# Kernel optimization log

Hardware: AMD Instinct MI355X
Metric: run time of the kernel (lower is better)

Reference implementation:

```python
import jax, jax.numpy as jnp
import numpy as np

N_S, N_T = 64, 32
N_EFF = N_S * N_T          # 2048
K_T1, K_T2 = 8, 8
BATCH = 16


def _orthonormal(key, n):
    q, _ = jnp.linalg.qr(jax.random.normal(key, (n, n), dtype=jnp.float32))
    return q.astype(jnp.float32)


def setup_inputs() -> dict:
    key = jax.random.key(0)
    ks = jax.random.split(key, 6)
    return {
        "s_effective_batch": jax.random.normal(ks[0], (BATCH, N_EFF), dtype=jnp.float32),
        "U_G": _orthonormal(ks[1], N_S),
        "U_P_T": _orthonormal(ks[2], N_T),
        "h0": jax.random.normal(ks[3], (N_EFF,), dtype=jnp.float32) * 0.01,
        "h_hat_1_coeffs": jax.random.normal(ks[4], (N_S, K_T1), dtype=jnp.float32) * 0.01,
        "H_hat_2_S": jax.random.normal(ks[5], (N_S, N_S), dtype=jnp.float32) * 0.01,
        "H_hat_2_T_coeffs": jax.random.normal(jax.random.fold_in(key, 7), (K_T2, K_T2), dtype=jnp.float32) * 0.01,
    }


def reference(s_effective_batch, U_G, U_P_T, h0, h_hat_1_coeffs, H_hat_2_S, H_hat_2_T_coeffs):
    # spatio-temporal basis via Kronecker product: [N_eff, N_eff]
    U_ST = jnp.kron(U_G, U_P_T)

    # GFT as in the module: s_hat = s @ U_ST
    s_hat = s_effective_batch @ U_ST                       # [B, N_eff]

    # linear (first-order Volterra) term
    Ub1 = U_P_T[:, :K_T1]                                  # [N_T, K1]
    full_h_hat_1 = (h_hat_1_coeffs @ Ub1.T).reshape(-1)    # [N_eff]
    z1 = (full_h_hat_1[None, :] * s_hat) @ U_ST            # iGFT as in module: @ U_ST

    # quadratic kernel H2 = kron(H2_S, Ub2 @ C @ Ub2^T)
    Ub2 = U_P_T[:, :K_T2]
    full_H2_T = Ub2 @ (H_hat_2_T_coeffs @ Ub2.T)           # [N_T, N_T]
    H2 = jnp.kron(H_hat_2_S, full_H2_T)                    # [N_eff, N_eff]

    # z2[b,i] = diag( U_ST (H2 * s_hat_b s_hat_b^T) U_ST^T )_i
    #         = sum_{k,l} B[b,i,k] H2[k,l] B[b,i,l], with B[b,i,k] = U_ST[i,k]*s_hat[b,k]
    B = U_ST[None, :, :] * s_hat[:, None, :]               # [B, N_eff, N_eff]
    z2 = jnp.einsum('bik,kl,bil->bi', B, H2, B)            # batched GEMM + row-reduce

    return h0[None, :] + z1 + z2
```

## Files before the change

### kernel.cpp

```cpp
#include <hip/hip_runtime.h>


typedef short  bf16x8 __attribute__((ext_vector_type(8)));
typedef float  f32x4  __attribute__((ext_vector_type(4)));

static __device__ __forceinline__ unsigned short f2bf(float f) {
  unsigned u = __float_as_uint(f);
  u = (u + 0x7fff + ((u >> 16) & 1)) >> 16;
  return (unsigned short)u;
}
static __device__ __forceinline__ float bf2f(unsigned short h) {
  return __uint_as_float(((unsigned)h) << 16);
}
static __device__ __forceinline__ float dot4(f32x4 a, f32x4 b) {
  return a.x * b.x + a.y * b.y + a.z * b.z + a.w * b.w;
}

__global__ __launch_bounds__(256) void volterra_one(
    const float* __restrict__ s, const float* __restrict__ UG,
    const float* __restrict__ UPT, const float* __restrict__ h0,
    const float* __restrict__ h1c, const float* __restrict__ HS,
    const float* __restrict__ Hc, float* __restrict__ out)
{
  const int b  = blockIdx.x >> 5;
  const int iT = blockIdx.x & 31;
  const int t  = threadIdx.x;
  const int w  = t >> 6;
  const int l  = t & 63;
  const int r  = l & 15;
  const int g  = l >> 4;

  __shared__ __align__(16) float sS[64][36];
  __shared__ __align__(16) float sT1E[2304];
  __shared__ __align__(16) unsigned short sUGh[4096];
  __shared__ __align__(16) unsigned short sUPTTh[32 * 40];
  __shared__ __align__(16) unsigned short sUPTTl[32 * 40];
  __shared__ float sUPT[32][33];
  __shared__ float sUhc[32 * 9];
  __shared__ float sh1c[512];
  __shared__ __align__(16) float wGm[8 * 36];
  __shared__ __align__(16) float wA[8 * 36];
  __shared__ __align__(16) float wQ[8 * 36];
  __shared__ __align__(16) float sGm[64][12];
  __shared__ __align__(16) float sA[64][12];
  __shared__ float wv[64];
  __shared__ float zp1[4][64];
  __shared__ float zpart[4][64];

  for (int o = t; o < 2048; o += 256) sS[o >> 5][o & 31] = s[b * 2048 + o];
  for (int o = t; o < 1024; o += 256) {
    const int k = o >> 5, c = o & 31;
    const float f = UPT[o];
    sUPT[k][c] = f;
    const unsigned short hi = f2bf(f);
    sUPTTh[c * 40 + k] = hi;
    sUPTTl[c * 40 + k] = f2bf(f - bf2f(hi));
  }
  for (int o = t; o < 4096; o += 256) {
    const int rr = o >> 6, c = o & 63;
    sUGh[rr * 64 + (c ^ ((rr & 7) << 3))] = f2bf(UG[o]);
  }
  for (int o = t; o < 512; o += 256) sh1c[o] = h1c[o];
  {
    const int k = t >> 3, p = t & 7;
    float a = 0.f;
    #pragma unroll
    for (int q = 0; q < 8; ++q) a += UPT[k * 32 + q] * Hc[q * 8 + p];
    sUhc[k * 9 + p] = a;
  }
  __syncthreads();

  {
    const int p = t >> 5, k = t & 31;
    const float uiT_row = sUPT[iT][k];
    const float uiT_col = sUPT[k][iT];
    wGm[p * 36 + k] = uiT_row * sUPT[k][p];
    wA [p * 36 + k] = uiT_row * sUhc[k * 9 + p];
    wQ [p * 36 + k] = uiT_col * sUPT[k][p];
  }
  {
    f32x4 acc0 = {0.f, 0.f, 0.f, 0.f}, acc1 = {0.f, 0.f, 0.f, 0.f};
    #pragma unroll
    for (int kc = 0; kc < 2; ++kc) {
      float av[8];
      #pragma unroll
      for (int j = 0; j < 8; ++j)
        av[j] = UG[(kc * 32 + g * 8 + j) * 64 + 16 * w + r];
      bf16x8 Ah, Al;
      #pragma unroll
      for (int j = 0; j < 8; ++j) {
        const unsigned short hi = f2bf(av[j]);
        Ah[j] = (short)hi;
        Al[j] = (short)f2bf(av[j] - bf2f(hi));
      }
      #pragma unroll
      for (int ct = 0; ct < 2; ++ct) {
        float bv[8];
        #pragma unroll
        for (int j = 0; j < 8; ++j)
          bv[j] = sS[kc * 32 + g * 8 + j][ct * 16 + r];
        bf16x8 Bh, Bl;
        #pragma unroll
        for (int j = 0; j < 8; ++j) {
          const unsigned short hi = f2bf(bv[j]);
          Bh[j] = (short)hi;
          Bl[j] = (short)f2bf(bv[j] - bf2f(hi));
        }
        f32x4& acc = ct ? acc1 : acc0;
        acc = __builtin_amdgcn_mfma_f32_16x16x32_bf16(Ah, Bh, acc, 0, 0, 0);
        acc = __builtin_amdgcn_mfma_f32_16x16x32_bf16(Ah, Bl, acc, 0, 0, 0);
        acc = __builtin_amdgcn_mfma_f32_16x16x32_bf16(Al, Bh, acc, 0, 0, 0);
      }
    }
    #pragma unroll
    for (int reg = 0; reg < 4; ++reg) {
      sT1E[(16 * w + 4 * g + reg) * 36 + r]      = acc0[reg];
      sT1E[(16 * w + 4 * g + reg) * 36 + 16 + r] = acc1[reg];
    }
  }
  __syncthreads();

  {
    f32x4 av0 = *(const f32x4*)&sT1E[(16 * w + r) * 36 + g * 8];
    f32x4 av1 = *(const f32x4*)&sT1E[(16 * w + r) * 36 + g * 8 + 4];
    float av[8] = {av0.x, av0.y, av0.z, av0.w, av1.x, av1.y, av1.z, av1.w};
    bf16x8 Ah, Al;
    #pragma unroll
    for (int j = 0; j < 8; ++j) {
      const unsigned short hi = f2bf(av[j]);
      Ah[j] = (short)hi;
      Al[j] = (short)f2bf(av[j] - bf2f(hi));
    }
    f32x4 acc0 = {0.f, 0.f, 0.f, 0.f}, acc1 = {0.f, 0.f, 0.f, 0.f};
    #pragma unroll
    for (int ct = 0; ct < 2; ++ct) {
      const bf16x8 Bh = *(const bf16x8*)&sUPTTh[(ct * 16 + r) * 40 + g * 8];
      const bf16x8 Bl = *(const bf16x8*)&sUPTTl[(ct * 16 + r) * 40 + g * 8];
      f32x4& acc = ct ? acc1 : acc0;
      acc = __builtin_amdgcn_mfma_f32_16x16x32_bf16(Ah, Bh, acc, 0, 0, 0);
      acc = __builtin_amdgcn_mfma_f32_16x16x32_bf16(Ah, Bl, acc, 0, 0, 0);
      acc = __builtin_amdgcn_mfma_f32_16x16x32_bf16(Al, Bh, acc, 0, 0, 0);
    }
    __syncthreads();
    #pragma unroll
    for (int reg = 0; reg < 4; ++reg) {
      sS[16 * w + 4 * g + reg][r]      = acc0[reg];
      sS[16 * w + 4 * g + reg][16 + r] = acc1[reg];
    }
  }
  __syncthreads();

  {
    const int kSa = t >> 3, p = t & 7;
    float g0 = 0.f, g1v = 0.f, a0 = 0.f, a1v = 0.f, q0 = 0.f, q1v = 0.f;
    #pragma unroll
    for (int c4 = 0; c4 < 8; ++c4) {
      const f32x4 w1 = *(const f32x4*)&wGm[p * 36 + c4 * 4];
      const f32x4 w2 = *(const f32x4*)&wA [p * 36 + c4 * 4];
      const f32x4 w3 = *(const f32x4*)&wQ [p * 36 + c4 * 4];
      const f32x4 x0 = *(const f32x4*)&sS[kSa][c4 * 4];
      const f32x4 x1 = *(const f32x4*)&sS[kSa + 32][c4 * 4];
      g0  += dot4(x0, w1); a0  += dot4(x0, w2); q0  += dot4(x0, w3);
      g1v += dot4(x1, w1); a1v += dot4(x1, w2); q1v += dot4(x1, w3);
    }
    sGm[kSa][p] = g0; sGm[kSa + 32][p] = g1v;
    sA [kSa][p] = a0; sA [kSa + 32][p] = a1v;
    float wv0 = sh1c[kSa * 8 + p] * q0;
    float wv1 = sh1c[(kSa + 32) * 8 + p] * q1v;
    wv0 += __shfl_xor(wv0, 1); wv0 += __shfl_xor(wv0, 2); wv0 += __shfl_xor(wv0, 4);
    wv1 += __shfl_xor(wv1, 1); wv1 += __shfl_xor(wv1, 2); wv1 += __shfl_xor(wv1, 4);
    if (p == 0) { wv[kSa] = wv0; wv[kSa + 32] = wv1; }
  }
  __syncthreads();

  {
    unsigned short* sEbf = (unsigned short*)sT1E;
    const f32x4 gr0 = *(const f32x4*)&sGm[l][0];
    const f32x4 gr1 = *(const f32x4*)&sGm[l][4];
    #pragma unroll 4
    for (int j = 0; j < 16; ++j) {
      const int kS = 4 * j + w;
      const f32x4 a0v = *(const f32x4*)&sA[kS][0];
      const f32x4 a1v = *(const f32x4*)&sA[kS][4];
      const float e = (dot4(a0v, gr0) + dot4(a1v, gr1)) * HS[kS * 64 + l];
      sEbf[kS * 64 + (l ^ ((kS & 7) << 3))] = f2bf(e);
    }
    const float wvl = wv[l];
    float part = 0.f;
    #pragma unroll
    for (int j = 0; j < 16; ++j) {
      const int kk = 16 * w + j;
      part += __shfl(wvl, kk) * UG[kk * 64 + l];
    }
    zp1[w][l] = part;
  }
  __syncthreads();

  {
    const unsigned short* sEbf = (const unsigned short*)sT1E;
    f32x4 acc[4];
    #pragma unroll
    for (int nt = 0; nt < 4; ++nt) acc[nt] = (f32x4){0.f, 0.f, 0.f, 0.f};
    #pragma unroll
    for (int ks = 0; ks < 2; ++ks) {
      const int kcol = g * 8 + ks * 32;
      const int rowA = 16 * w + r;
      const bf16x8 ah = *(const bf16x8*)&sEbf[rowA * 64 + (kcol ^ ((rowA & 7) << 3))];
      #pragma unroll
      for (int nt = 0; nt < 4; ++nt) {
        const int rowB = 16 * nt + r;
        const bf16x8 bh = *(const bf16x8*)&sUGh[rowB * 64 + (kcol ^ ((rowB & 7) << 3))];
        acc[nt] = __builtin_amdgcn_mfma_f32_16x16x32_bf16(ah, bh, acc[nt], 0, 0, 0);
      }
    }
    #pragma unroll
    for (int nt = 0; nt < 4; ++nt) {
      float zp = 0.f;
      #pragma unroll
      for (int reg = 0; reg < 4; ++reg) {
        const int kS = 16 * w + 4 * g + reg;
        const int iS = 16 * nt + r;
        zp += bf2f(sUGh[iS * 64 + (kS ^ ((iS & 7) << 3))]) * acc[nt][reg];
      }
      zp += __shfl_xor(zp, 16);
      zp += __shfl_xor(zp, 32);
      if (g == 0) zpart[w][16 * nt + r] = zp;
    }
  }
  __syncthreads();

  if (t < 64) {
    const float z2 = zpart[0][t] + zpart[1][t] + zpart[2][t] + zpart[3][t];
    const float z1 = zp1[0][t] + zp1[1][t] + zp1[2][t] + zp1[3][t];
    const int col = t * 32 + iT;
    out[b * 2048 + col] = h0[col] + z1 + z2;
  }
}

extern "C" void kernel_launch(void* const* d_in, const int* in_sizes, int n_in,
                              void* d_out, int out_size, void* d_ws, size_t ws_size,
                              hipStream_t stream) {
  const float* s   = (const float*)d_in[0];
  const float* UG  = (const float*)d_in[1];
  const float* UPT = (const float*)d_in[2];
  const float* h0  = (const float*)d_in[3];
  const float* h1c = (const float*)d_in[4];
  const float* HS  = (const float*)d_in[5];
  const float* Hc  = (const float*)d_in[6];
  float* out = (float*)d_out;

  volterra_one<<<512, 256, 0, stream>>>(s, UG, UPT, h0, h1c, HS, Hc, out);
}
```

Baseline: 14.78 us.

## Process two temporal indices per block to share GFT work across halves

Each block now handles two iT columns with 512 threads, halving the grid to 256 blocks. The shared s_hat computation (two MFMA GEMM stages) is split across 8 waves instead of recomputed per iT. Later stages run per side in parallel. Global loads are vectorized, and HS is staged in shared memory. This reduces redundant per-block prologue and GEMM work, at the cost of more LDS per block and fewer blocks (256 on a ~256-CU part, so about one block per CU).

```diff
diff --git a/kernel.cpp b/kernel.cpp
--- a/kernel.cpp
+++ b/kernel.cpp
@@ -3,66 +3,80 @@
 
 typedef short  bf16x8 __attribute__((ext_vector_type(8)));
 typedef float  f32x4  __attribute__((ext_vector_type(4)));
-
-static __device__ __forceinline__ unsigned short f2bf(float f) {
+typedef unsigned short u16;
+
+static __device__ __forceinline__ u16 f2bf(float f) {
   unsigned u = __float_as_uint(f);
   u = (u + 0x7fff + ((u >> 16) & 1)) >> 16;
-  return (unsigned short)u;
-}
-static __device__ __forceinline__ float bf2f(unsigned short h) {
+  return (u16)u;
+}
+static __device__ __forceinline__ float bf2f(u16 h) {
   return __uint_as_float(((unsigned)h) << 16);
 }
 static __device__ __forceinline__ float dot4(f32x4 a, f32x4 b) {
   return a.x * b.x + a.y * b.y + a.z * b.z + a.w * b.w;
 }
 
-__global__ __launch_bounds__(256) void volterra_one(
+__global__ __launch_bounds__(512) void volterra_one(
     const float* __restrict__ s, const float* __restrict__ UG,
     const float* __restrict__ UPT, const float* __restrict__ h0,
     const float* __restrict__ h1c, const float* __restrict__ HS,
     const float* __restrict__ Hc, float* __restrict__ out)
 {
-  const int b  = blockIdx.x >> 5;
-  const int iT = blockIdx.x & 31;
-  const int t  = threadIdx.x;
-  const int w  = t >> 6;
-  const int l  = t & 63;
-  const int r  = l & 15;
-  const int g  = l >> 4;
+  const int b   = blockIdx.x >> 4;
+  const int iT0 = (blockIdx.x & 15) << 1;
+  const int t   = threadIdx.x;
+  const int w   = t >> 6;
+  const int l   = t & 63;
+  const int r   = l & 15;
+  const int g   = l >> 4;
 
   __shared__ __align__(16) float sS[64][36];
-  __shared__ __align__(16) float sT1E[2304];
-  __shared__ __align__(16) unsigned short sUGh[4096];
-  __shared__ __align__(16) unsigned short sUPTTh[32 * 40];
-  __shared__ __align__(16) unsigned short sUPTTl[32 * 40];
-  __shared__ float sUPT[32][33];
+  __shared__ __align__(16) float sT1[64][36];
+  __shared__ __align__(16) u16   sUGh[4096];
+  __shared__ __align__(16) u16   sUPTTh[32 * 40];
+  __shared__ __align__(16) u16   sUPTTl[32 * 40];
+  __shared__ __align__(16) float sUPT[32][36];
+  __shared__ __align__(16) float sHS[64][68];
   __shared__ float sUhc[32 * 9];
-  __shared__ float sh1c[512];
-  __shared__ __align__(16) float wGm[8 * 36];
-  __shared__ __align__(16) float wA[8 * 36];
-  __shared__ __align__(16) float wQ[8 * 36];
-  __shared__ __align__(16) float sGm[64][12];
-  __shared__ __align__(16) float sA[64][12];
-  __shared__ float wv[64];
-  __shared__ float zp1[4][64];
-  __shared__ float zpart[4][64];
-
-  for (int o = t; o < 2048; o += 256) sS[o >> 5][o & 31] = s[b * 2048 + o];
-  for (int o = t; o < 1024; o += 256) {
-    const int k = o >> 5, c = o & 31;
-    const float f = UPT[o];
-    sUPT[k][c] = f;
-    const unsigned short hi = f2bf(f);
-    sUPTTh[c * 40 + k] = hi;
-    sUPTTl[c * 40 + k] = f2bf(f - bf2f(hi));
-  }
-  for (int o = t; o < 4096; o += 256) {
-    const int rr = o >> 6, c = o & 63;
-    sUGh[rr * 64 + (c ^ ((rr & 7) << 3))] = f2bf(UG[o]);
-  }
-  for (int o = t; o < 512; o += 256) sh1c[o] = h1c[o];
-  {
-    const int k = t >> 3, p = t & 7;
+  __shared__ __align__(16) float wGm[2][8 * 36], wA[2][8 * 36], wQ[2][8 * 36];
+  __shared__ __align__(16) float sGm[2][64][12], sA[2][64][12];
+  __shared__ __align__(16) u16   sE[2][4096];
+  __shared__ float wv[2][64];
+  __shared__ float zp1[2][4][64];
+  __shared__ float zpart[2][4][64];
+
+  {
+    const f32x4 v = ((const f32x4*)(s + b * 2048))[t];
+    *(f32x4*)&sS[t >> 3][(t & 7) * 4] = v;
+  }
+  #pragma unroll
+  for (int o4 = t, it = 0; it < 2; ++it, o4 += 512) {
+    const int rr = o4 >> 4, c0 = (o4 & 15) * 4;
+    const f32x4 v = ((const f32x4*)UG)[o4];
+    short4 h;
+    h.x = (short)f2bf(v.x); h.y = (short)f2bf(v.y);
+    h.z = (short)f2bf(v.z); h.w = (short)f2bf(v.w);
+    *(short4*)&sUGh[rr * 64 + (c0 ^ ((rr & 7) << 3))] = h;
+  }
+  #pragma unroll
+  for (int o4 = t, it = 0; it < 2; ++it, o4 += 512) {
+    const int rr = o4 >> 4, c0 = (o4 & 15) * 4;
+    *(f32x4*)&sHS[rr][c0] = ((const f32x4*)HS)[o4];
+  }
+  if (t < 256) {
+    const int k = t >> 3, c4 = t & 7;
+    const f32x4 v = ((const f32x4*)UPT)[t];
+    *(f32x4*)&sUPT[k][c4 * 4] = v;
+    float arr[4] = {v.x, v.y, v.z, v.w};
+    #pragma unroll
+    for (int i = 0; i < 4; ++i) {
+      const int c = 4 * c4 + i;
+      const u16 hi = f2bf(arr[i]);
+      sUPTTh[c * 40 + k] = hi;
+      sUPTTl[c * 40 + k] = f2bf(arr[i] - bf2f(hi));
+    }
+    const int p = t & 7;
     float a = 0.f;
     #pragma unroll
     for (int q = 0; q < 8; ++q) a += UPT[k * 32 + q] * Hc[q * 8 + p];
@@ -71,141 +85,125 @@
   __syncthreads();
 
   {
-    const int p = t >> 5, k = t & 31;
-    const float uiT_row = sUPT[iT][k];
-    const float uiT_col = sUPT[k][iT];
-    wGm[p * 36 + k] = uiT_row * sUPT[k][p];
-    wA [p * 36 + k] = uiT_row * sUhc[k * 9 + p];
-    wQ [p * 36 + k] = uiT_col * sUPT[k][p];
-  }
-  {
-    f32x4 acc0 = {0.f, 0.f, 0.f, 0.f}, acc1 = {0.f, 0.f, 0.f, 0.f};
+    const int side = t >> 8, p = (t >> 5) & 7, k = t & 31;
+    const int iTs = iT0 + side;
+    const float m1 = sUPT[iTs][k];
+    const float m3 = sUPT[k][iTs];
+    const float m2 = sUPT[k][p];
+    wGm[side][p * 36 + k] = m1 * m2;
+    wA [side][p * 36 + k] = m1 * sUhc[k * 9 + p];
+    wQ [side][p * 36 + k] = m3 * m2;
+  }
+  {
+    const int band = w >> 1, ct = w & 1;
+    f32x4 acc = {0.f, 0.f, 0.f, 0.f};
     #pragma unroll
     for (int kc = 0; kc < 2; ++kc) {
-      float av[8];
+      float av[8], bv[8];
       #pragma unroll
       for (int j = 0; j < 8; ++j)
-        av[j] = UG[(kc * 32 + g * 8 + j) * 64 + 16 * w + r];
-      bf16x8 Ah, Al;
+        av[j] = UG[(kc * 32 + g * 8 + j) * 64 + 16 * band + r];
+      #pragma unroll
+      for (int j = 0; j < 8; ++j)
+        bv[j] = sS[kc * 32 + g * 8 + j][ct * 16 + r];
+      bf16x8 Ah, Al, Bh, Bl;
       #pragma unroll
       for (int j = 0; j < 8; ++j) {
-        const unsigned short hi = f2bf(av[j]);
-        Ah[j] = (short)hi;
-        Al[j] = (short)f2bf(av[j] - bf2f(hi));
+        u16 h = f2bf(av[j]);
+        Ah[j] = (short)h; Al[j] = (short)f2bf(av[j] - bf2f(h));
+        h = f2bf(bv[j]);
+        Bh[j] = (short)h; Bl[j] = (short)f2bf(bv[j] - bf2f(h));
       }
-      #pragma unroll
-      for (int ct = 0; ct < 2; ++ct) {
-        float bv[8];
-        #pragma unroll
-        for (int j = 0; j < 8; ++j)
-          bv[j] = sS[kc * 32 + g * 8 + j][ct * 16 + r];
-        bf16x8 Bh, Bl;
-        #pragma unroll
-        for (int j = 0; j < 8; ++j) {
-          const unsigned short hi = f2bf(bv[j]);
-          Bh[j] = (short)hi;
-          Bl[j] = (short)f2bf(bv[j] - bf2f(hi));
-        }
-        f32x4& acc = ct ? acc1 : acc0;
-        acc = __builtin_amdgcn_mfma_f32_16x16x32_bf16(Ah, Bh, acc, 0, 0, 0);
-        acc = __builtin_amdgcn_mfma_f32_16x16x32_bf16(Ah, Bl, acc, 0, 0, 0);
-        acc = __builtin_amdgcn_mfma_f32_16x16x32_bf16(Al, Bh, acc, 0, 0, 0);
-      }
-    }
-    #pragma unroll
-    for (int reg = 0; reg < 4; ++reg) {
-      sT1E[(16 * w + 4 * g + reg) * 36 + r]      = acc0[reg];
-      sT1E[(16 * w + 4 * g + reg) * 36 + 16 + r] = acc1[reg];
-    }
-  }
-  __syncthreads();
-
-  {
-    f32x4 av0 = *(const f32x4*)&sT1E[(16 * w + r) * 36 + g * 8];
-    f32x4 av1 = *(const f32x4*)&sT1E[(16 * w + r) * 36 + g * 8 + 4];
-    float av[8] = {av0.x, av0.y, av0.z, av0.w, av1.x, av1.y, av1.z, av1.w};
-    bf16x8 Ah, Al;
-    #pragma unroll
-    for (int j = 0; j < 8; ++j) {
-      const unsigned short hi = f2bf(av[j]);
-      Ah[j] = (short)hi;
-      Al[j] = (short)f2bf(av[j] - bf2f(hi));
-    }
-    f32x4 acc0 = {0.f, 0.f, 0.f, 0.f}, acc1 = {0.f, 0.f, 0.f, 0.f};
-    #pragma unroll
-    for (int ct = 0; ct < 2; ++ct) {
-      const bf16x8 Bh = *(const bf16x8*)&sUPTTh[(ct * 16 + r) * 40 + g * 8];
-      const bf16x8 Bl = *(const bf16x8*)&sUPTTl[(ct * 16 + r) * 40 + g * 8];
-      f32x4& acc = ct ? acc1 : acc0;
       acc = __builtin_amdgcn_mfma_f32_16x16x32_bf16(Ah, Bh, acc, 0, 0, 0);
       acc = __builtin_amdgcn_mfma_f32_16x16x32_bf16(Ah, Bl, acc, 0, 0, 0);
       acc = __builtin_amdgcn_mfma_f32_16x16x32_bf16(Al, Bh, acc, 0, 0, 0);
     }
-    __syncthreads();
-    #pragma unroll
-    for (int reg = 0; reg < 4; ++reg) {
-      sS[16 * w + 4 * g + reg][r]      = acc0[reg];
-      sS[16 * w + 4 * g + reg][16 + r] = acc1[reg];
-    }
-  }
-  __syncthreads();
-
-  {
-    const int kSa = t >> 3, p = t & 7;
+    #pragma unroll
+    for (int reg = 0; reg < 4; ++reg)
+      sT1[16 * band + 4 * g + reg][ct * 16 + r] = acc[reg];
+  }
+  __syncthreads();
+
+  {
+    const int band = w >> 1, ct = w & 1;
+    const f32x4 a0 = *(const f32x4*)&sT1[16 * band + r][g * 8];
+    const f32x4 a1 = *(const f32x4*)&sT1[16 * band + r][g * 8 + 4];
+    float av[8] = {a0.x, a0.y, a0.z, a0.w, a1.x, a1.y, a1.z, a1.w};
+    bf16x8 Ah, Al;
+    #pragma unroll
+    for (int j = 0; j < 8; ++j) {
+      const u16 h = f2bf(av[j]);
+      Ah[j] = (short)h; Al[j] = (short)f2bf(av[j] - bf2f(h));
+    }
+    const bf16x8 Bh = *(const bf16x8*)&sUPTTh[(ct * 16 + r) * 40 + g * 8];
+    const bf16x8 Bl = *(const bf16x8*)&sUPTTl[(ct * 16 + r) * 40 + g * 8];
+    f32x4 acc = {0.f, 0.f, 0.f, 0.f};
+    acc = __builtin_amdgcn_mfma_f32_16x16x32_bf16(Ah, Bh, acc, 0, 0, 0);
+    acc = __builtin_amdgcn_mfma_f32_16x16x32_bf16(Ah, Bl, acc, 0, 0, 0);
+    acc = __builtin_amdgcn_mfma_f32_16x16x32_bf16(Al, Bh, acc, 0, 0, 0);
+    #pragma unroll
+    for (int reg = 0; reg < 4; ++reg)
+      sS[16 * band + 4 * g + reg][ct * 16 + r] = acc[reg];
+  }
+  __syncthreads();
+
+  {
+    const int side = t >> 8, ts = t & 255;
+    const int kSa = ts >> 3, p = ts & 7;
     float g0 = 0.f, g1v = 0.f, a0 = 0.f, a1v = 0.f, q0 = 0.f, q1v = 0.f;
     #pragma unroll
     for (int c4 = 0; c4 < 8; ++c4) {
-      const f32x4 w1 = *(const f32x4*)&wGm[p * 36 + c4 * 4];
-      const f32x4 w2 = *(const f32x4*)&wA [p * 36 + c4 * 4];
-      const f32x4 w3 = *(const f32x4*)&wQ [p * 36 + c4 * 4];
+      const f32x4 w1 = *(const f32x4*)&wGm[side][p * 36 + c4 * 4];
+      const f32x4 w2 = *(const f32x4*)&wA [side][p * 36 + c4 * 4];
+      const f32x4 w3 = *(const f32x4*)&wQ [side][p * 36 + c4 * 4];
       const f32x4 x0 = *(const f32x4*)&sS[kSa][c4 * 4];
       const f32x4 x1 = *(const f32x4*)&sS[kSa + 32][c4 * 4];
       g0  += dot4(x0, w1); a0  += dot4(x0, w2); q0  += dot4(x0, w3);
       g1v += dot4(x1, w1); a1v += dot4(x1, w2); q1v += dot4(x1, w3);
     }
-    sGm[kSa][p] = g0; sGm[kSa + 32][p] = g1v;
-    sA [kSa][p] = a0; sA [kSa + 32][p] = a1v;
-    float wv0 = sh1c[kSa * 8 + p] * q0;
-    float wv1 = sh1c[(kSa + 32) * 8 + p] * q1v;
+    sGm[side][kSa][p] = g0; sGm[side][kSa + 32][p] = g1v;
+    sA [side][kSa][p] = a0; sA [side][kSa + 32][p] = a1v;
+    float wv0 = h1c[kSa * 8 + p] * q0;
+    float wv1 = h1c[(kSa + 32) * 8 + p] * q1v;
     wv0 += __shfl_xor(wv0, 1); wv0 += __shfl_xor(wv0, 2); wv0 += __shfl_xor(wv0, 4);
     wv1 += __shfl_xor(wv1, 1); wv1 += __shfl_xor(wv1, 2); wv1 += __shfl_xor(wv1, 4);
-    if (p == 0) { wv[kSa] = wv0; wv[kSa + 32] = wv1; }
-  }
-  __syncthreads();
-
-  {
-    unsigned short* sEbf = (unsigned short*)sT1E;
-    const f32x4 gr0 = *(const f32x4*)&sGm[l][0];
-    const f32x4 gr1 = *(const f32x4*)&sGm[l][4];
+    if (p == 0) { wv[side][kSa] = wv0; wv[side][kSa + 32] = wv1; }
+  }
+  __syncthreads();
+
+  {
+    const int side = t >> 8, sub = (t >> 6) & 3;
+    const f32x4 gr0 = *(const f32x4*)&sGm[side][l][0];
+    const f32x4 gr1 = *(const f32x4*)&sGm[side][l][4];
     #pragma unroll 4
     for (int j = 0; j < 16; ++j) {
-      const int kS = 4 * j + w;
-      const f32x4 a0v = *(const f32x4*)&sA[kS][0];
-      const f32x4 a1v = *(const f32x4*)&sA[kS][4];
-      const float e = (dot4(a0v, gr0) + dot4(a1v, gr1)) * HS[kS * 64 + l];
-      sEbf[kS * 64 + (l ^ ((kS & 7) << 3))] = f2bf(e);
-    }
-    const float wvl = wv[l];
+      const int kS = 4 * j + sub;
+      const f32x4 a0v = *(const f32x4*)&sA[side][kS][0];
+      const f32x4 a1v = *(const f32x4*)&sA[side][kS][4];
+      const float e = (dot4(a0v, gr0) + dot4(a1v, gr1)) * sHS[kS][l];
+      sE[side][kS * 64 + (l ^ ((kS & 7) << 3))] = f2bf(e);
+    }
+    const float wvl = wv[side][l];
     float part = 0.f;
     #pragma unroll
     for (int j = 0; j < 16; ++j) {
-      const int kk = 16 * w + j;
+      const int kk = 16 * sub + j;
       part += __shfl(wvl, kk) * UG[kk * 64 + l];
     }
-    zp1[w][l] = part;
-  }
-  __syncthreads();
-
-  {
-    const unsigned short* sEbf = (const unsigned short*)sT1E;
+    zp1[side][sub][l] = part;
+  }
+  __syncthreads();
+
+  {
+    const int side = t >> 8, sub = (t >> 6) & 3;
     f32x4 acc[4];
     #pragma unroll
     for (int nt = 0; nt < 4; ++nt) acc[nt] = (f32x4){0.f, 0.f, 0.f, 0.f};
     #pragma unroll
     for (int ks = 0; ks < 2; ++ks) {
       const int kcol = g * 8 + ks * 32;
-      const int rowA = 16 * w + r;
-      const bf16x8 ah = *(const bf16x8*)&sEbf[rowA * 64 + (kcol ^ ((rowA & 7) << 3))];
+      const int rowA = 16 * sub + r;
+      const bf16x8 ah = *(const bf16x8*)&sE[side][rowA * 64 + (kcol ^ ((rowA & 7) << 3))];
       #pragma unroll
       for (int nt = 0; nt < 4; ++nt) {
         const int rowB = 16 * nt + r;
@@ -218,21 +216,24 @@
       float zp = 0.f;
       #pragma unroll
       for (int reg = 0; reg < 4; ++reg) {
-        const int kS = 16 * w + 4 * g + reg;
+        const int kS = 16 * sub + 4 * g + reg;
         const int iS = 16 * nt + r;
         zp += bf2f(sUGh[iS * 64 + (kS ^ ((iS & 7) << 3))]) * acc[nt][reg];
       }
       zp += __shfl_xor(zp, 16);
       zp += __shfl_xor(zp, 32);
-      if (g == 0) zpart[w][16 * nt + r] = zp;
-    }
-  }
-  __syncthreads();
-
-  if (t < 64) {
-    const float z2 = zpart[0][t] + zpart[1][t] + zpart[2][t] + zpart[3][t];
-    const float z1 = zp1[0][t] + zp1[1][t] + zp1[2][t] + zp1[3][t];
-    const int col = t * 32 + iT;
+      if (g == 0) zpart[side][sub][16 * nt + r] = zp;
+    }
+  }
+  __syncthreads();
+
+  if (t < 128) {
+    const int side = t >> 6, c = t & 63;
+    const float z2 = zpart[side][0][c] + zpart[side][1][c] +
+                     zpart[side][2][c] + zpart[side][3][c];
+    const float z1 = zp1[side][0][c] + zp1[side][1][c] +
+                     zp1[side][2][c] + zp1[side][3][c];
+    const int col = c * 32 + iT0 + side;
     out[b * 2048 + col] = h0[col] + z1 + z2;
   }
 }
@@ -249,5 +250,5 @@
   const float* Hc  = (const float*)d_in[6];
   float* out = (float*)d_out;
 
-  volterra_one<<<512, 256, 0, stream>>>(s, UG, UPT, h0, h1c, HS, Hc, out);
-}
+  volterra_one<<<256, 512, 0, stream>>>(s, UG, UPT, h0, h1c, HS, Hc, out);
+}
```

After: 15.04 us. Within noise of the previous version (+1.8%).
